# Kernel optimization log

Measured on AMD Instinct MI355X. Metric: run time of the kernel, lower is better.

Reference implementation:

```python
import jax, jax.numpy as jnp
import numpy as np

N = 20000      # nodes
E = 320000     # edges
F = 128        # feat_dim
N_RBF = 20
CUTOFF = 5.0


def setup_inputs() -> dict:
    key = jax.random.key(0)
    ks = jax.random.split(key, 12)
    h_i = jax.random.normal(ks[0], (N, F), dtype=jnp.float32)
    v_i = jax.random.normal(ks[1], (N, F, 3), dtype=jnp.float32)
    # distances in (0, cutoff); keep strictly > 0 to avoid div-by-zero in sinc basis
    d_ij = (jax.random.uniform(ks[2], (E,), dtype=jnp.float32) * 0.98 + 0.01) * CUTOFF
    r = jax.random.normal(ks[3], (E, 3), dtype=jnp.float32)
    unit_r_ij = r / jnp.linalg.norm(r, axis=-1, keepdims=True)
    nbrs = jax.random.randint(ks[4], (E, 2), 0, N, dtype=jnp.int64)
    # params: layers = Dense(F->F, swish) then Dense(F->3F); dist_embed dense: n_rbf -> 3F
    s1 = 1.0 / np.sqrt(F)
    W1 = jax.random.uniform(ks[5], (F, F), jnp.float32, -s1, s1)
    b1 = jax.random.uniform(ks[6], (F,), jnp.float32, -s1, s1)
    W2 = jax.random.uniform(ks[7], (F, 3 * F), jnp.float32, -s1, s1)
    b2 = jax.random.uniform(ks[8], (3 * F,), jnp.float32, -s1, s1)
    sr = 1.0 / np.sqrt(N_RBF)
    Wr = jax.random.uniform(ks[9], (N_RBF, 3 * F), jnp.float32, -sr, sr)
    br = jax.random.uniform(ks[10], (3 * F,), jnp.float32, -sr, sr)
    return {"h_i": h_i, "v_i": v_i, "d_ij": d_ij, "unit_r_ij": unit_r_ij,
            "nbrs": nbrs, "W1": W1, "b1": b1, "W2": W2, "b2": b2, "Wr": Wr, "br": br}


def _dist_embed(d, Wr, br):
    # PaiNN sinc-like radial basis: sin(n*pi*d/cutoff)/d, n=1..N_RBF
    n = jnp.arange(1, N_RBF + 1, dtype=d.dtype)
    rbf = jnp.sin(n[None, :] * jnp.pi * d[:, None] / CUTOFF) / d[:, None]  # [E, N_RBF]
    # cosine cutoff envelope
    fcut = 0.5 * (jnp.cos(jnp.pi * d / CUTOFF) + 1.0) * (d < CUTOFF)       # [E]
    return (rbf @ Wr + br) * fcut[:, None]                                  # [E, 3F]


def reference(h_i, v_i, d_ij, unit_r_ij, nbrs, W1, b1, W2, b2, Wr, br):
    # phi = Dense(swish) -> Dense : [N, 3F]
    phi = jax.nn.silu(h_i @ W1 + b1) @ W2 + b2
    src = nbrs[:, 1]
    dst = nbrs[:, 0]
    edge_inv = phi[src] * _dist_embed(d_ij, Wr, br)          # [E, 3F]
    edge_inv = edge_inv.reshape(edge_inv.shape[0], 3, F)     # [E, 3, F]
    f1, f2, f3 = edge_inv[:, 0], edge_inv[:, 1], edge_inv[:, 2]
    # dv: [E, F, 3]
    dv = f1[:, :, None] * unit_r_ij[:, None, :] + f2[:, :, None] * v_i[src]
    dh_i = jax.ops.segment_sum(f3, dst, num_segments=N)      # [N, F]
    dv_i = jax.ops.segment_sum(dv, dst, num_segments=N)      # [N, F, 3]
    return (dh_i, dv_i)
```

## Files before the change

### kernel.cpp

```cpp
#include <hip/hip_runtime.h>
#include <math.h>

#define F 128
#define THREEF 384
#define N_RBF 20
#define CUTOFF 5.0f
#define CAP 64
#define TLDS_STRIDE 136

typedef __bf16 bf16x8 __attribute__((ext_vector_type(8)));
typedef float  f32x4  __attribute__((ext_vector_type(4)));

__global__ __launch_bounds__(256) void wcast_kernel(
    const float* __restrict__ W1, const float* __restrict__ W2,
    __bf16* __restrict__ W1T, __bf16* __restrict__ W2T)
{
    const int idx = blockIdx.x * 256 + threadIdx.x;
    if (idx < 128 * 128) {
        const int n = idx >> 7, k = idx & 127;
        W1T[idx] = (__bf16)W1[k * F + n];
    }
    if (idx < 384 * 128) {
        const int n = idx >> 7, k = idx & 127;
        W2T[idx] = (__bf16)W2[k * THREEF + n];
    }
}

__global__ __launch_bounds__(256) void mlp_mfma_kernel(
    const float* __restrict__ h,
    const __bf16* __restrict__ W1T,
    const float* __restrict__ b1,
    const __bf16* __restrict__ W2T,
    const float* __restrict__ b2,
    float* __restrict__ phi, int N)
{
    __shared__ __bf16 t_lds[4][16 * TLDS_STRIDE];

    const int wave = threadIdx.x >> 6;
    const int lane = threadIdx.x & 63;
    const int m    = lane & 15;
    const int quad = lane >> 4;
    const int node0 = blockIdx.x * 64 + wave * 16;
    if (node0 >= N) return;

    bf16x8 a1[4];
    #pragma unroll
    for (int kb = 0; kb < 4; ++kb) {
        const float* hp = h + (size_t)(node0 + m) * F + kb * 32 + quad * 8;
        const float4 x0 = *(const float4*)hp;
        const float4 x1 = *(const float4*)(hp + 4);
        bf16x8 a;
        a[0] = (__bf16)x0.x; a[1] = (__bf16)x0.y;
        a[2] = (__bf16)x0.z; a[3] = (__bf16)x0.w;
        a[4] = (__bf16)x1.x; a[5] = (__bf16)x1.y;
        a[6] = (__bf16)x1.z; a[7] = (__bf16)x1.w;
        a1[kb] = a;
    }

    #pragma unroll
    for (int ct = 0; ct < 8; ++ct) {
        f32x4 acc = {0.0f, 0.0f, 0.0f, 0.0f};
        #pragma unroll
        for (int kb = 0; kb < 4; ++kb) {
            const bf16x8 b =
                *(const bf16x8*)(W1T + (size_t)(ct * 16 + m) * F + kb * 32 + quad * 8);
            acc = __builtin_amdgcn_mfma_f32_16x16x32_bf16(a1[kb], b, acc, 0, 0, 0);
        }
        const int col = ct * 16 + m;
        const float bb = b1[col];
        #pragma unroll
        for (int reg = 0; reg < 4; ++reg) {
            const float x = acc[reg] + bb;
            const float s = x / (1.0f + __expf(-x));
            t_lds[wave][(quad * 4 + reg) * TLDS_STRIDE + col] = (__bf16)s;
        }
    }

    bf16x8 a2[4];
    #pragma unroll
    for (int kb = 0; kb < 4; ++kb)
        a2[kb] = *(const bf16x8*)&t_lds[wave][m * TLDS_STRIDE + kb * 32 + quad * 8];

    #pragma unroll
    for (int ct = 0; ct < 24; ++ct) {
        f32x4 acc = {0.0f, 0.0f, 0.0f, 0.0f};
        #pragma unroll
        for (int kb = 0; kb < 4; ++kb) {
            const bf16x8 b =
                *(const bf16x8*)(W2T + (size_t)(ct * 16 + m) * F + kb * 32 + quad * 8);
            acc = __builtin_amdgcn_mfma_f32_16x16x32_bf16(a2[kb], b, acc, 0, 0, 0);
        }
        const int col   = ct * 16 + m;
        const int plane = col >> 7;
        const int fc    = col & 127;
        const float bb  = b2[col];
        float* pp = phi + (size_t)plane * N * F + fc;
        #pragma unroll
        for (int reg = 0; reg < 4; ++reg) {
            const int row = quad * 4 + reg;
            pp[(size_t)(node0 + row) * F] = acc[reg] + bb;
        }
    }
}

__global__ __launch_bounds__(256) void wrt_kernel(
    const float* __restrict__ Wr, float* __restrict__ WrT)
{
    const int idx = blockIdx.x * 256 + threadIdx.x;
    if (idx >= 5 * 3 * 128) return;
    const int f  = idx & 127;
    const int c  = (idx >> 7) % 3;
    const int n4 = idx / (3 * 128);
    float4 v;
    v.x = Wr[(4 * n4 + 0) * THREEF + c * 128 + f];
    v.y = Wr[(4 * n4 + 1) * THREEF + c * 128 + f];
    v.z = Wr[(4 * n4 + 2) * THREEF + c * 128 + f];
    v.w = Wr[(4 * n4 + 3) * THREEF + c * 128 + f];
    ((float4*)WrT)[idx] = v;
}

__global__ __launch_bounds__(256) void build_kernel(
    const float* __restrict__ d_ij, const float* __restrict__ unit_r,
    const int* __restrict__ nbrs, int* __restrict__ cnt,
    int* __restrict__ eid, float* __restrict__ pack, int E)
{
    int e = blockIdx.x * 256 + threadIdx.x;
    if (e >= E) return;
    const int2 nb = ((const int2*)nbrs)[e];
    const int dst = nb.x;
    const int src = nb.y;
    const int slot = atomicAdd(&cnt[dst], 1);
    if (slot < CAP) eid[dst * CAP + slot] = e;

    const float d = d_ij[e];
    const float x = (float)M_PI * d * (1.0f / CUTOFF);
    float sx, cx;
    __sincosf(x, &sx, &cx);
    const float fcut = (d < CUTOFF) ? 0.5f * (cx + 1.0f) : 0.0f;
    float4 q0, q1;
    q0.x = sx * fcut / d;
    q0.y = 2.0f * cx;
    q0.z = fcut;
    q0.w = unit_r[3 * e + 0];
    q1.x = unit_r[3 * e + 1];
    q1.y = unit_r[3 * e + 2];
    q1.z = __int_as_float(src);
    q1.w = 0.0f;
    float4* pk = (float4*)(pack + (size_t)e * 8);
    pk[0] = q0;
    pk[1] = q1;
}

__global__ __launch_bounds__(128) void gather_kernel(
    const float* __restrict__ phi,
    const float* __restrict__ v_i,
    const float* __restrict__ WrT,
    const float* __restrict__ br,
    const int*   __restrict__ cnt,
    const int*   __restrict__ eid,
    const float* __restrict__ pack,
    float* __restrict__ dh,
    float* __restrict__ dv,
    int N)
{
    const int node = blockIdx.x;
    const int f    = threadIdx.x;

    const float br0 = br[f], br1 = br[f + 128], br2 = br[f + 256];

    const int deg0 = cnt[node];
    const int deg  = deg0 < CAP ? deg0 : CAP;
    const int* my_eid = eid + node * CAP;

    const float* phi0 = phi;
    const float* phi1 = phi + (size_t)N * F;
    const float* phi2 = phi + (size_t)2 * N * F;
    const float4* wT  = (const float4*)WrT;

    float dh_acc = 0.0f, dv0 = 0.0f, dv1 = 0.0f, dv2 = 0.0f;

    for (int i = 0; i < deg; ++i) {
        const int e = __builtin_amdgcn_readfirstlane(my_eid[i]);
        const float* pk = pack + (size_t)e * 8;
        const float s1   = pk[0];
        const float twoc = pk[1];
        const float fcut = pk[2];
        const float ux   = pk[3];
        const float uy   = pk[4];
        const float uz   = pk[5];
        const int src = __builtin_amdgcn_readfirstlane(__float_as_int(pk[6]));

        float a0 = br0 * fcut, a1 = br1 * fcut, a2 = br2 * fcut;
        float rp = 0.0f, rc = s1;
        #pragma unroll
        for (int n4 = 0; n4 < 5; ++n4) {
            const float4 w0 = wT[(n4 * 3 + 0) * 128 + f];
            const float4 w1 = wT[(n4 * 3 + 1) * 128 + f];
            const float4 w2 = wT[(n4 * 3 + 2) * 128 + f];
            #pragma unroll
            for (int k = 0; k < 4; ++k) {
                const float wa = ((const float*)&w0)[k];
                const float wb = ((const float*)&w1)[k];
                const float wc = ((const float*)&w2)[k];
                a0 = fmaf(rc, wa, a0);
                a1 = fmaf(rc, wb, a1);
                a2 = fmaf(rc, wc, a2);
                const float rn = fmaf(twoc, rc, -rp);
                rp = rc;
                rc = rn;
            }
        }

        const float f1 = phi0[(size_t)src * F + f] * a0;
        const float f2 = phi1[(size_t)src * F + f] * a1;
        const float f3 = phi2[(size_t)src * F + f] * a2;

        dh_acc += f3;

        const float* vs = v_i + (size_t)src * THREEF + 3 * f;
        dv0 = fmaf(f1, ux, fmaf(f2, vs[0], dv0));
        dv1 = fmaf(f1, uy, fmaf(f2, vs[1], dv1));
        dv2 = fmaf(f1, uz, fmaf(f2, vs[2], dv2));
    }

    dh[(size_t)node * F + f] = dh_acc;
    float* dvp = dv + (size_t)node * THREEF + 3 * f;
    dvp[0] = dv0;
    dvp[1] = dv1;
    dvp[2] = dv2;
}

extern "C" void kernel_launch(void* const* d_in, const int* in_sizes, int n_in,
                              void* d_out, int out_size, void* d_ws, size_t ws_size,
                              hipStream_t stream) {
    const float* h_i    = (const float*)d_in[0];
    const float* v_i    = (const float*)d_in[1];
    const float* d_ij   = (const float*)d_in[2];
    const float* unit_r = (const float*)d_in[3];
    const int*   nbrs   = (const int*)  d_in[4];
    const float* W1     = (const float*)d_in[5];
    const float* b1     = (const float*)d_in[6];
    const float* W2     = (const float*)d_in[7];
    const float* b2     = (const float*)d_in[8];
    const float* Wr     = (const float*)d_in[9];
    const float* br     = (const float*)d_in[10];

    const int N = in_sizes[0] / F;
    const int E = in_sizes[2];

    float* dh = (float*)d_out;
    float* dv = dh + (size_t)N * F;

    float*  phi  = (float*)d_ws;
    float*  pack = phi + (size_t)3 * N * F;
    float*  WrT  = pack + (size_t)E * 8;
    int*    cnt  = (int*)(WrT + 5 * 3 * 128 * 4);
    int*    eid  = cnt + N;
    __bf16* W1T  = (__bf16*)(eid + (size_t)N * CAP);
    __bf16* W2T  = W1T + 128 * 128;

    hipMemsetAsync(cnt, 0, (size_t)N * sizeof(int), stream);

    wcast_kernel<<<192, 256, 0, stream>>>(W1, W2, W1T, W2T);
    mlp_mfma_kernel<<<(N + 63) / 64, 256, 0, stream>>>(h_i, W1T, b1, W2T, b2,
                                                       phi, N);
    wrt_kernel<<<8, 256, 0, stream>>>(Wr, WrT);
    build_kernel<<<(E + 255) / 256, 256, 0, stream>>>(d_ij, unit_r, nbrs, cnt,
                                                      eid, pack, E);
    gather_kernel<<<N, 128, 0, stream>>>(phi, v_i, WrT, br, cnt, eid, pack,
                                         dh, dv, N);
}
```

Before: 299.3 us.

## Scatter edge packs into per-node slots, fuse prep kernels, stage packs in LDS

The build step now writes each edge's packed record directly into a per-destination slot array, which removes the eid indirection. The weight-cast, Wr transpose and edge build kernels are merged into one launch. The gather kernel handles two nodes per 256-thread block and loads each node's contiguous pack rows into shared memory once, so the loop no longer does dependent scalar global loads. In exchange the pack buffer grows to N*CAP records, and N/2 blocks assumes N is even.

New measurement: 294.9 us. No clear change (-1.5%).

```diff
diff --git a/kernel.cpp b/kernel.cpp
--- a/kernel.cpp
+++ b/kernel.cpp
@@ -11,18 +11,66 @@
 typedef __bf16 bf16x8 __attribute__((ext_vector_type(8)));
 typedef float  f32x4  __attribute__((ext_vector_type(4)));
 
-__global__ __launch_bounds__(256) void wcast_kernel(
+__global__ __launch_bounds__(256) void prep_kernel(
+    const float* __restrict__ d_ij, const float* __restrict__ unit_r,
+    const int* __restrict__ nbrs,
     const float* __restrict__ W1, const float* __restrict__ W2,
-    __bf16* __restrict__ W1T, __bf16* __restrict__ W2T)
+    const float* __restrict__ Wr,
+    int* __restrict__ cnt, float* __restrict__ pack,
+    __bf16* __restrict__ W1T, __bf16* __restrict__ W2T,
+    float* __restrict__ WrT, int E, int EB)
 {
-    const int idx = blockIdx.x * 256 + threadIdx.x;
-    if (idx < 128 * 128) {
-        const int n = idx >> 7, k = idx & 127;
-        W1T[idx] = (__bf16)W1[k * F + n];
-    }
-    if (idx < 384 * 128) {
-        const int n = idx >> 7, k = idx & 127;
-        W2T[idx] = (__bf16)W2[k * THREEF + n];
+    const int tid = threadIdx.x;
+    const int b   = blockIdx.x;
+
+    if (b < EB) {
+        const int e = b * 256 + tid;
+        if (e >= E) return;
+        const int2 nb = ((const int2*)nbrs)[e];
+        const int dst = nb.x;
+        const int src = nb.y;
+        const int slot = atomicAdd(&cnt[dst], 1);
+        if (slot >= CAP) return;
+
+        const float d = d_ij[e];
+        const float x = (float)M_PI * d * (1.0f / CUTOFF);
+        float sx, cx;
+        __sincosf(x, &sx, &cx);
+        const float fcut = (d < CUTOFF) ? 0.5f * (cx + 1.0f) : 0.0f;
+        float4 q0, q1;
+        q0.x = sx * fcut / d;
+        q0.y = 2.0f * cx;
+        q0.z = fcut;
+        q0.w = unit_r[3 * e + 0];
+        q1.x = unit_r[3 * e + 1];
+        q1.y = unit_r[3 * e + 2];
+        q1.z = __int_as_float(src);
+        q1.w = 0.0f;
+        float4* pk = (float4*)(pack + ((size_t)dst * CAP + slot) * 8);
+        pk[0] = q0;
+        pk[1] = q1;
+    } else if (b < EB + 256) {
+        const int idx = (b - EB) * 256 + tid;
+        if (idx < 128 * 128) {
+            const int n = idx >> 7, k = idx & 127;
+            W1T[idx] = (__bf16)W1[k * F + n];
+        }
+        if (idx < 384 * 128) {
+            const int n = idx >> 7, k = idx & 127;
+            W2T[idx] = (__bf16)W2[k * THREEF + n];
+        }
+    } else {
+        const int idx = (b - EB - 256) * 256 + tid;
+        if (idx >= 5 * 3 * 128) return;
+        const int f  = idx & 127;
+        const int c  = (idx >> 7) % 3;
+        const int n4 = idx / (3 * 128);
+        float4 v;
+        v.x = Wr[(4 * n4 + 0) * THREEF + c * 128 + f];
+        v.y = Wr[(4 * n4 + 1) * THREEF + c * 128 + f];
+        v.z = Wr[(4 * n4 + 2) * THREEF + c * 128 + f];
+        v.w = Wr[(4 * n4 + 3) * THREEF + c * 128 + f];
+        ((float4*)WrT)[idx] = v;
     }
 }
 
@@ -103,74 +151,34 @@
     }
 }
 
-__global__ __launch_bounds__(256) void wrt_kernel(
-    const float* __restrict__ Wr, float* __restrict__ WrT)
-{
-    const int idx = blockIdx.x * 256 + threadIdx.x;
-    if (idx >= 5 * 3 * 128) return;
-    const int f  = idx & 127;
-    const int c  = (idx >> 7) % 3;
-    const int n4 = idx / (3 * 128);
-    float4 v;
-    v.x = Wr[(4 * n4 + 0) * THREEF + c * 128 + f];
-    v.y = Wr[(4 * n4 + 1) * THREEF + c * 128 + f];
-    v.z = Wr[(4 * n4 + 2) * THREEF + c * 128 + f];
-    v.w = Wr[(4 * n4 + 3) * THREEF + c * 128 + f];
-    ((float4*)WrT)[idx] = v;
-}
-
-__global__ __launch_bounds__(256) void build_kernel(
-    const float* __restrict__ d_ij, const float* __restrict__ unit_r,
-    const int* __restrict__ nbrs, int* __restrict__ cnt,
-    int* __restrict__ eid, float* __restrict__ pack, int E)
-{
-    int e = blockIdx.x * 256 + threadIdx.x;
-    if (e >= E) return;
-    const int2 nb = ((const int2*)nbrs)[e];
-    const int dst = nb.x;
-    const int src = nb.y;
-    const int slot = atomicAdd(&cnt[dst], 1);
-    if (slot < CAP) eid[dst * CAP + slot] = e;
-
-    const float d = d_ij[e];
-    const float x = (float)M_PI * d * (1.0f / CUTOFF);
-    float sx, cx;
-    __sincosf(x, &sx, &cx);
-    const float fcut = (d < CUTOFF) ? 0.5f * (cx + 1.0f) : 0.0f;
-    float4 q0, q1;
-    q0.x = sx * fcut / d;
-    q0.y = 2.0f * cx;
-    q0.z = fcut;
-    q0.w = unit_r[3 * e + 0];
-    q1.x = unit_r[3 * e + 1];
-    q1.y = unit_r[3 * e + 2];
-    q1.z = __int_as_float(src);
-    q1.w = 0.0f;
-    float4* pk = (float4*)(pack + (size_t)e * 8);
-    pk[0] = q0;
-    pk[1] = q1;
-}
-
-__global__ __launch_bounds__(128) void gather_kernel(
+__global__ __launch_bounds__(256) void gather_kernel(
     const float* __restrict__ phi,
     const float* __restrict__ v_i,
     const float* __restrict__ WrT,
     const float* __restrict__ br,
     const int*   __restrict__ cnt,
-    const int*   __restrict__ eid,
     const float* __restrict__ pack,
     float* __restrict__ dh,
     float* __restrict__ dv,
     int N)
 {
-    const int node = blockIdx.x;
-    const int f    = threadIdx.x;
-
-    const float br0 = br[f], br1 = br[f + 128], br2 = br[f + 256];
+    __shared__ float4 s_pack[2][CAP * 2];
+
+    const int tid  = threadIdx.x;
+    const int half = tid >> 7;
+    const int f    = tid & 127;
+    const int node = blockIdx.x * 2 + half;
 
     const int deg0 = cnt[node];
     const int deg  = deg0 < CAP ? deg0 : CAP;
-    const int* my_eid = eid + node * CAP;
+
+    {
+        const float4* src = (const float4*)(pack + (size_t)node * CAP * 8);
+        if (f < 2 * deg) s_pack[half][f] = src[f];
+    }
+    __syncthreads();
+
+    const float br0 = br[f], br1 = br[f + 128], br2 = br[f + 256];
 
     const float* phi0 = phi;
     const float* phi1 = phi + (size_t)N * F;
@@ -180,15 +188,14 @@
     float dh_acc = 0.0f, dv0 = 0.0f, dv1 = 0.0f, dv2 = 0.0f;
 
     for (int i = 0; i < deg; ++i) {
-        const int e = __builtin_amdgcn_readfirstlane(my_eid[i]);
-        const float* pk = pack + (size_t)e * 8;
-        const float s1   = pk[0];
-        const float twoc = pk[1];
-        const float fcut = pk[2];
-        const float ux   = pk[3];
-        const float uy   = pk[4];
-        const float uz   = pk[5];
-        const int src = __builtin_amdgcn_readfirstlane(__float_as_int(pk[6]));
+        const float* q = (const float*)&s_pack[half][2 * i];
+        const float s1   = q[0];
+        const float twoc = q[1];
+        const float fcut = q[2];
+        const float ux   = q[3];
+        const float uy   = q[4];
+        const float uz   = q[5];
+        const int src = __builtin_amdgcn_readfirstlane(__float_as_int(q[6]));
 
         float a0 = br0 * fcut, a1 = br1 * fcut, a2 = br2 * fcut;
         float rp = 0.0f, rc = s1;
@@ -253,20 +260,19 @@
 
     float*  phi  = (float*)d_ws;
     float*  pack = phi + (size_t)3 * N * F;
-    float*  WrT  = pack + (size_t)E * 8;
+    float*  WrT  = pack + (size_t)N * CAP * 8;
     int*    cnt  = (int*)(WrT + 5 * 3 * 128 * 4);
-    int*    eid  = cnt + N;
-    __bf16* W1T  = (__bf16*)(eid + (size_t)N * CAP);
+    __bf16* W1T  = (__bf16*)(cnt + N);
     __bf16* W2T  = W1T + 128 * 128;
 
+    const int EB = (E + 255) / 256;
+
     hipMemsetAsync(cnt, 0, (size_t)N * sizeof(int), stream);
 
-    wcast_kernel<<<192, 256, 0, stream>>>(W1, W2, W1T, W2T);
+    prep_kernel<<<EB + 256 + 8, 256, 0, stream>>>(
+        d_ij, unit_r, nbrs, W1, W2, Wr, cnt, pack, W1T, W2T, WrT, E, EB);
     mlp_mfma_kernel<<<(N + 63) / 64, 256, 0, stream>>>(h_i, W1T, b1, W2T, b2,
                                                        phi, N);
-    wrt_kernel<<<8, 256, 0, stream>>>(Wr, WrT);
-    build_kernel<<<(E + 255) / 256, 256, 0, stream>>>(d_ij, unit_r, nbrs, cnt,
-                                                      eid, pack, E);
-    gather_kernel<<<N, 128, 0, stream>>>(phi, v_i, WrT, br, cnt, eid, pack,
-                                         dh, dv, N);
-}
+    gather_kernel<<<N / 2, 256, 0, stream>>>(phi, v_i, WrT, br, cnt, pack,
+                                             dh, dv, N);
+}
```
